# Performance work log

Measured on AMD Instinct MI355X. Metric: run time of the kernel, lower is better.

Reference implementation:

```python
import jax, jax.numpy as jnp
import numpy as np

N_NODES = 100000
N_EDGES = 1600000
NUM_FEATURES = 128
HIDDEN = 64
NUM_CLASSES = 16


def setup_inputs() -> dict:
    key = jax.random.key(0)
    k1, k2, k3, k4 = jax.random.split(key, 4)
    x = jax.random.normal(k1, (N_NODES, NUM_FEATURES), dtype=jnp.float32)
    edge_index = jax.random.randint(k2, (2, N_EDGES), 0, N_NODES, dtype=jnp.int64)
    # Glorot-ish scaled weights ([in, out] layout; PyG stores [out,in] but math is x @ W)
    W1 = jax.random.normal(k3, (NUM_FEATURES, HIDDEN), dtype=jnp.float32) * (1.0 / np.sqrt(NUM_FEATURES))
    W2 = jax.random.normal(k4, (HIDDEN, NUM_CLASSES), dtype=jnp.float32) * (1.0 / np.sqrt(HIDDEN))
    return {"x": x, "edge_index": edge_index, "W1": W1, "W2": W2}


def _gcn_conv(x, edge_index, W):
    # GCNConv(add_self_loops=False, bias=False): linear then sym-normalized scatter-add.
    n = x.shape[0]
    row, col = edge_index[0], edge_index[1]  # source -> target
    h = x @ W  # [N, out]
    # degree from unit edge weights scattered on target nodes
    deg = jax.ops.segment_sum(jnp.ones(row.shape[0], dtype=h.dtype), col, num_segments=n)
    deg_inv_sqrt = jnp.where(deg > 0, jax.lax.rsqrt(jnp.maximum(deg, 1.0)), 0.0)
    norm = deg_inv_sqrt[row] * deg_inv_sqrt[col]  # [E]
    msg = h[row] * norm[:, None]  # gather + scale, [E, out]
    return jax.ops.segment_sum(msg, col, num_segments=n)  # scatter-add to targets


def reference(x, edge_index, W1, W2):
    h = _gcn_conv(x, edge_index, W1)
    h = _gcn_conv(h, edge_index, W2)
    return jax.nn.log_softmax(h, axis=1)
```

## Files before the change

### kernel.cpp

```cpp
#include <hip/hip_runtime.h>
#include <hip/hip_bf16.h>
#include <hip/hip_fp16.h>


#define STRIDE 48
#define BCAP   3072


__global__ __launch_bounds__(512) void k_bucket(const int* __restrict__ ei,
                                                const void* __restrict__ xv,
                                                const void* __restrict__ W1v,
                                                const void* __restrict__ W2v,
                                                int* __restrict__ flags,
                                                float* __restrict__ W12,
                                                int* __restrict__ bcnt,
                                                int* __restrict__ buf,
                                                int e, int n, int nb) {
    __shared__ int hist[1024];
    __shared__ int basec[1024];
    __shared__ float wtmp[2048];
    __shared__ int sraw, sbad;
    int t = threadIdx.x;
    int b = blockIdx.x;

    if (t == 0) { sraw = 0; sbad = 0; }
    for (int i = t; i < nb; i += 512) hist[i] = 0;
    __syncthreads();

    {
        int i = b * 4096 + t;
        if (i < e && ei[2 * (size_t)i + 1] != 0) atomicOr(&sraw, 1);
    }
    if (b < 8) {
        const unsigned short* xs = (const unsigned short*)xv;
        int bad = 0;
        for (int i = t; i < 1024; i += 512) {
            unsigned ex2 = (xs[i] >> 7) & 0xFF;
            if (ex2 >= 0x90) bad = 1;
        }
        if (bad) atomicOr(&sbad, 1);
    }
    __syncthreads();
    int raw = sraw ? 0 : 1;

    if (b < 8) {
        bool f32 = sbad != 0;
        if (f32) {
            const float* W1 = (const float*)W1v;
            const float* W2 = (const float*)W2v;
            for (int i = t; i < 1024; i += 512) {
                wtmp[i] = W1[b * 1024 + i];
                wtmp[1024 + i] = W2[i];
            }
        } else {
            const __hip_bfloat16* W1 = (const __hip_bfloat16*)W1v;
            const __hip_bfloat16* W2 = (const __hip_bfloat16*)W2v;
            for (int i = t; i < 1024; i += 512) {
                wtmp[i] = __bfloat162float(W1[b * 1024 + i]);
                wtmp[1024 + i] = __bfloat162float(W2[i]);
            }
        }
    }

    int e0 = b * 4096;
    int bk[8], rec[8];
#pragma unroll
    for (int j = 0; j < 8; ++j) {
        int i = e0 + j * 512 + t;
        bk[j] = -1;
        if (i < e) {
            int r, c;
            if (raw) {
                r = ((const int2*)ei)[(size_t)i].x;
                c = ((const int2*)ei)[(size_t)e + i].x;
            } else {
                r = ei[i];
                c = ei[(size_t)e + i];
            }
            if ((unsigned)c < (unsigned)n && (unsigned)r < (unsigned)n) {
                bk[j] = c >> 7;
                rec[j] = ((c & 127) << 17) | r;
                atomicAdd(&hist[bk[j]], 1);
            }
        }
    }
    __syncthreads();

    if (b < 8 && t < 256) {
        int kl = t >> 4, c = t & 15;
        float acc = 0.0f;
#pragma unroll 8
        for (int f = 0; f < 64; ++f) acc += wtmp[kl * 64 + f] * wtmp[1024 + f * 16 + c];
        W12[(16 * b + kl) * 16 + c] = acc;
        if (b == 0 && t == 0) { flags[0] = sbad; flags[1] = raw; }
    }

    for (int i = t; i < nb; i += 512) {
        int h = hist[i];
        basec[i] = h ? atomicAdd(&bcnt[i], h) : 0;
    }
    __syncthreads();
#pragma unroll
    for (int j = 0; j < 8; ++j) {
        if (bk[j] >= 0) {
            int slot = atomicAdd(&basec[bk[j]], 1);
            if (slot < BCAP) buf[(size_t)bk[j] * BCAP + slot] = rec[j];
        }
    }
}


__global__ __launch_bounds__(256) void k_csr(const int* __restrict__ bcnt,
                                             const int* __restrict__ buf,
                                             int* __restrict__ cnt,
                                             int* __restrict__ csr, int n) {
    __shared__ int lcnt[128];
    __shared__ int lcsr[128 * STRIDE];
    int t = threadIdx.x;
    int b = blockIdx.x;
    if (t < 128) lcnt[t] = 0;
    int4 zero4 = {0, 0, 0, 0};
    for (int i = t; i < 128 * STRIDE / 4; i += 256) ((int4*)lcsr)[i] = zero4;
    __syncthreads();

    int m = bcnt[b];
    if (m > BCAP) m = BCAP;
    for (int i = t; i < m; i += 256) {
        int rec = buf[(size_t)b * BCAP + i];
        int cl = rec >> 17;
        int r = rec & 0x1FFFF;
        int slot = atomicAdd(&lcnt[cl], 1);
        if (slot < STRIDE) lcsr[cl * STRIDE + slot] = r;
    }
    __syncthreads();
    int node = (b << 7) + t;
    if (t < 128 && node < n) cnt[node] = lcnt[t];
    const int4* src = (const int4*)lcsr;
    int4* dst = (int4*)csr + (size_t)b * (128 * STRIDE / 4);
    for (int i = t; i < 128 * STRIDE / 4; i += 256) dst[i] = src[i];
}


__global__ __launch_bounds__(512) void k_z(const void* __restrict__ xv,
                                           const float* __restrict__ W12,
                                           const int* __restrict__ flags,
                                           const int* __restrict__ cnt,
                                           __half* __restrict__ z, int n) {
    __shared__ float part[4][128][17];
    int t = threadIdx.x;
    int b = blockIdx.x;
    int node_l = t & 127;
    int kq = t >> 7;
    int node0 = (b << 7) + node_l;
    int node = node0 < n ? node0 : n - 1;

    float acc[16];
#pragma unroll
    for (int c = 0; c < 16; ++c) acc[c] = 0.0f;

    if (flags[0]) {
        const float4* x4 = (const float4*)xv + (size_t)node * 32 + kq * 8;
#pragma unroll
        for (int j = 0; j < 8; ++j) {
            float4 v = x4[j];
            float xk[4] = {v.x, v.y, v.z, v.w};
#pragma unroll
            for (int q = 0; q < 4; ++q) {
                const float* w = &W12[(kq * 32 + j * 4 + q) * 16];
                float xx = xk[q];
#pragma unroll
                for (int c = 0; c < 16; ++c) acc[c] += xx * w[c];
            }
        }
    } else {
        const uint4* x4 = (const uint4*)xv + (size_t)node * 16 + kq * 4;
#pragma unroll
        for (int j = 0; j < 4; ++j) {
            uint4 v = x4[j];
            float xk[8];
            xk[0] = __uint_as_float(v.x << 16);
            xk[1] = __uint_as_float(v.x & 0xffff0000u);
            xk[2] = __uint_as_float(v.y << 16);
            xk[3] = __uint_as_float(v.y & 0xffff0000u);
            xk[4] = __uint_as_float(v.z << 16);
            xk[5] = __uint_as_float(v.z & 0xffff0000u);
            xk[6] = __uint_as_float(v.w << 16);
            xk[7] = __uint_as_float(v.w & 0xffff0000u);
#pragma unroll
            for (int q = 0; q < 8; ++q) {
                const float* w = &W12[(kq * 32 + j * 8 + q) * 16];
                float xx = xk[q];
#pragma unroll
                for (int c = 0; c < 16; ++c) acc[c] += xx * w[c];
            }
        }
    }

#pragma unroll
    for (int c = 0; c < 16; ++c) part[kq][node_l][c] = acc[c];
    __syncthreads();

    int nl2 = t >> 2;
    int cg = (t & 3) * 4;
    int node2 = (b << 7) + nl2;
    if (node2 < n) {
        float s0 = part[0][nl2][cg + 0] + part[1][nl2][cg + 0] + part[2][nl2][cg + 0] + part[3][nl2][cg + 0];
        float s1 = part[0][nl2][cg + 1] + part[1][nl2][cg + 1] + part[2][nl2][cg + 1] + part[3][nl2][cg + 1];
        float s2 = part[0][nl2][cg + 2] + part[1][nl2][cg + 2] + part[2][nl2][cg + 2] + part[3][nl2][cg + 2];
        float s3 = part[0][nl2][cg + 3] + part[1][nl2][cg + 3] + part[2][nl2][cg + 3] + part[3][nl2][cg + 3];
        int deg = cnt[node2];
        float di = (deg > 0) ? rsqrtf((float)deg) : 0.0f;
        __half2 h0 = __halves2half2(__float2half(s0 * di), __float2half(s1 * di));
        __half2 h1 = __halves2half2(__float2half(s2 * di), __float2half(s3 * di));
        uint2 u;
        u.x = *(unsigned*)&h0;
        u.y = *(unsigned*)&h1;
        ((uint2*)(z + (size_t)node2 * 16))[t & 3] = u;
    }
}


__global__ __launch_bounds__(256) void k_agg1b(const int* __restrict__ cnt,
                                               const int* __restrict__ csr,
                                               const __half* __restrict__ z,
                                               __half* __restrict__ z2, int n) {
    int t = threadIdx.x;
    int wid = t >> 6, lane = t & 63;
    int half = lane >> 5, l5 = lane & 31;
    int node0 = blockIdx.x * 8 + wid * 2 + half;
    int node = node0 < n ? node0 : n - 1;
    int id  = csr[(size_t)node * STRIDE + l5];
    int id2 = csr[(size_t)node * STRIDE + 32 + (l5 & 15)];
    int deg = cnt[node];
    float di = (deg > 0) ? rsqrtf((float)deg) : 0.0f;
    int m = deg < STRIDE ? deg : STRIDE;
    int sub = l5 >> 3, f2 = l5 & 7;
    int base = half << 5;
    const __half2* zp = (const __half2*)z;
    float ax = 0.0f, ay = 0.0f;
#pragma unroll
    for (int j = 0; j < 24; j += 4) {
        int s = __shfl(id, base + j + sub);
        float2 v = __half22float2(zp[(size_t)s * 8 + f2]);
        bool ok = (j + sub) < m;
        ax += ok ? v.x : 0.0f;
        ay += ok ? v.y : 0.0f;
    }
    for (int j = 24; j < m; j += 4) {
        int sidx = j + sub;
        int s = (j < 32) ? __shfl(id, base + sidx)
                         : __shfl(id2, base + (sidx & 15));
        if (sidx < m) {
            float2 v = __half22float2(zp[(size_t)s * 8 + f2]);
            ax += v.x;
            ay += v.y;
        }
    }
    ax += __shfl_xor(ax, 8);  ay += __shfl_xor(ay, 8);
    ax += __shfl_xor(ax, 16); ay += __shfl_xor(ay, 16);
    float s2 = di * di;
    if (node0 < n && l5 < 8)
        ((__half2*)z2)[(size_t)node * 8 + l5] =
            __halves2half2(__float2half(ax * s2), __float2half(ay * s2));
}


__global__ __launch_bounds__(256) void k_agg2b(const int* __restrict__ cnt,
                                               const int* __restrict__ csr,
                                               const __half* __restrict__ z2,
                                               const int* __restrict__ flags,
                                               void* __restrict__ outv, int n) {
    int t = threadIdx.x;
    int wid = t >> 6, lane = t & 63;
    int half = lane >> 5, l5 = lane & 31;
    int node0 = blockIdx.x * 8 + wid * 2 + half;
    int node = node0 < n ? node0 : n - 1;
    int id  = csr[(size_t)node * STRIDE + l5];
    int id2 = csr[(size_t)node * STRIDE + 32 + (l5 & 15)];
    int deg = cnt[node];
    float di = (deg > 0) ? rsqrtf((float)deg) : 0.0f;
    int m = deg < STRIDE ? deg : STRIDE;
    int sub = l5 >> 3, f2 = l5 & 7;
    int base = half << 5;
    const __half2* zp = (const __half2*)z2;
    float ax = 0.0f, ay = 0.0f;
#pragma unroll
    for (int j = 0; j < 24; j += 4) {
        int s = __shfl(id, base + j + sub);
        float2 v = __half22float2(zp[(size_t)s * 8 + f2]);
        bool ok = (j + sub) < m;
        ax += ok ? v.x : 0.0f;
        ay += ok ? v.y : 0.0f;
    }
    for (int j = 24; j < m; j += 4) {
        int sidx = j + sub;
        int s = (j < 32) ? __shfl(id, base + sidx)
                         : __shfl(id2, base + (sidx & 15));
        if (sidx < m) {
            float2 v = __half22float2(zp[(size_t)s * 8 + f2]);
            ax += v.x;
            ay += v.y;
        }
    }
    ax += __shfl_xor(ax, 8);  ay += __shfl_xor(ay, 8);
    ax += __shfl_xor(ax, 16); ay += __shfl_xor(ay, 16);
    float vx = ax * di, vy = ay * di;
    float mx = fmaxf(vx, vy);
#pragma unroll
    for (int d = 1; d <= 4; d <<= 1) mx = fmaxf(mx, __shfl_xor(mx, d));
    float es = __expf(vx - mx) + __expf(vy - mx);
#pragma unroll
    for (int d = 1; d <= 4; d <<= 1) es += __shfl_xor(es, d);
    float ls = __logf(es);
    float rx = vx - mx - ls, ry = vy - mx - ls;
    if (node0 < n && l5 < 8) {
        if (flags[0]) {
            float2 r; r.x = rx; r.y = ry;
            ((float2*)outv)[(size_t)node * 8 + l5] = r;
        } else {
            __hip_bfloat162 hh;
            hh.x = __float2bfloat16(rx);
            hh.y = __float2bfloat16(ry);
            ((__hip_bfloat162*)outv)[(size_t)node * 8 + l5] = hh;
        }
    }
}


extern "C" void kernel_launch(void* const* d_in, const int* in_sizes, int n_in,
                              void* d_out, int out_size, void* d_ws, size_t ws_size,
                              hipStream_t stream) {
    const int F = 128, C = 16;
    int n = in_sizes[0] / F;
    int e = in_sizes[1] / 2;
    int nb = (n + 127) >> 7;

    const void* x = d_in[0];
    const int* ei = (const int*)d_in[1];
    const void* W1 = d_in[2];
    const void* W2 = d_in[3];

    char* p = (char*)d_ws;
    auto carve = [&](size_t bytes) {
        char* r = p;
        p += (bytes + 255) & ~(size_t)255;
        return r;
    };
    int*    flags = (int*)  carve(256);
    int*    bcnt  = (int*)  carve((size_t)nb * 4);
    int*    cnt   = (int*)  carve((size_t)n * 4);
    float*  W12   = (float*)carve(128 * 16 * 4);
    int*    csr   = (int*)  carve(((size_t)nb * 128 * STRIDE + 64) * 4);
    __half* z     = (__half*)carve((size_t)n * C * 2);
    size_t buf_sz = (size_t)nb * BCAP * 4;
    size_t z2_sz = (size_t)n * C * 2;
    char* regionB = carve(buf_sz > z2_sz ? buf_sz : z2_sz);
    int*    buf = (int*)regionB;
    __half* z2  = (__half*)regionB;
    (void)ws_size;

    int gb_bucket = (e + 4095) / 4096;
    if (gb_bucket < 8) gb_bucket = 8;

    hipMemsetAsync(bcnt, 0, (size_t)nb * 4, stream);
    k_bucket<<<gb_bucket, 512, 0, stream>>>(ei, x, W1, W2, flags, W12, bcnt, buf, e, n, nb);
    k_csr<<<nb, 256, 0, stream>>>(bcnt, buf, cnt, csr, n);
    k_z<<<nb, 512, 0, stream>>>(x, W12, flags, cnt, z, n);
    k_agg1b<<<(n + 7) / 8, 256, 0, stream>>>(cnt, csr, z, z2, n);
    k_agg2b<<<(n + 7) / 8, 256, 0, stream>>>(cnt, csr, z2, flags, d_out, n);
}
```

Baseline: 193.1 us.

## Fuse projection kernel into CSR build and halve bucket block size

Merges the node projection (x @ W1W2 scaled by deg^-1/2) into the per-bucket CSR kernel, so the degree comes from shared memory and one kernel launch plus the cnt round-trip are removed. W12 is staged in shared memory. Each node now uses two threads that combine results with a shuffle, instead of four that reduce through shared memory. The bucketing kernel moves to 256-thread blocks covering 2048 edges each, which doubles the grid. The trade-off is heavier per-thread work and more register and shared-memory use in the fused kernel, with fewer threads per node for the x loads.

```diff
diff --git a/kernel.cpp b/kernel.cpp
--- a/kernel.cpp
+++ b/kernel.cpp
@@ -7,7 +7,7 @@
 #define BCAP   3072
 
 
-__global__ __launch_bounds__(512) void k_bucket(const int* __restrict__ ei,
+__global__ __launch_bounds__(256) void k_bucket(const int* __restrict__ ei,
                                                 const void* __restrict__ xv,
                                                 const void* __restrict__ W1v,
                                                 const void* __restrict__ W2v,
@@ -24,17 +24,17 @@
     int b = blockIdx.x;
 
     if (t == 0) { sraw = 0; sbad = 0; }
-    for (int i = t; i < nb; i += 512) hist[i] = 0;
+    for (int i = t; i < nb; i += 256) hist[i] = 0;
     __syncthreads();
 
     {
-        int i = b * 4096 + t;
+        int i = b * 2048 + t;
         if (i < e && ei[2 * (size_t)i + 1] != 0) atomicOr(&sraw, 1);
     }
     if (b < 8) {
         const unsigned short* xs = (const unsigned short*)xv;
         int bad = 0;
-        for (int i = t; i < 1024; i += 512) {
+        for (int i = t; i < 1024; i += 256) {
             unsigned ex2 = (xs[i] >> 7) & 0xFF;
             if (ex2 >= 0x90) bad = 1;
         }
@@ -48,25 +48,25 @@
         if (f32) {
             const float* W1 = (const float*)W1v;
             const float* W2 = (const float*)W2v;
-            for (int i = t; i < 1024; i += 512) {
+            for (int i = t; i < 1024; i += 256) {
                 wtmp[i] = W1[b * 1024 + i];
                 wtmp[1024 + i] = W2[i];
             }
         } else {
             const __hip_bfloat16* W1 = (const __hip_bfloat16*)W1v;
             const __hip_bfloat16* W2 = (const __hip_bfloat16*)W2v;
-            for (int i = t; i < 1024; i += 512) {
+            for (int i = t; i < 1024; i += 256) {
                 wtmp[i] = __bfloat162float(W1[b * 1024 + i]);
                 wtmp[1024 + i] = __bfloat162float(W2[i]);
             }
         }
     }
 
-    int e0 = b * 4096;
+    int e0 = b * 2048;
     int bk[8], rec[8];
 #pragma unroll
     for (int j = 0; j < 8; ++j) {
-        int i = e0 + j * 512 + t;
+        int i = e0 + j * 256 + t;
         bk[j] = -1;
         if (i < e) {
             int r, c;
@@ -86,7 +86,7 @@
     }
     __syncthreads();
 
-    if (b < 8 && t < 256) {
+    if (b < 8) {
         int kl = t >> 4, c = t & 15;
         float acc = 0.0f;
 #pragma unroll 8
@@ -95,7 +95,7 @@
         if (b == 0 && t == 0) { flags[0] = sbad; flags[1] = raw; }
     }
 
-    for (int i = t; i < nb; i += 512) {
+    for (int i = t; i < nb; i += 256) {
         int h = hist[i];
         basec[i] = h ? atomicAdd(&bcnt[i], h) : 0;
     }
@@ -110,17 +110,23 @@
 }
 
 
-__global__ __launch_bounds__(256) void k_csr(const int* __restrict__ bcnt,
-                                             const int* __restrict__ buf,
-                                             int* __restrict__ cnt,
-                                             int* __restrict__ csr, int n) {
+__global__ __launch_bounds__(256) void k_csr_z(const int* __restrict__ bcnt,
+                                               const int* __restrict__ buf,
+                                               const void* __restrict__ xv,
+                                               const float* __restrict__ W12,
+                                               const int* __restrict__ flags,
+                                               int* __restrict__ cnt,
+                                               int* __restrict__ csr,
+                                               __half* __restrict__ z, int n) {
     __shared__ int lcnt[128];
     __shared__ int lcsr[128 * STRIDE];
+    __shared__ float ws[2048];
     int t = threadIdx.x;
     int b = blockIdx.x;
     if (t < 128) lcnt[t] = 0;
     int4 zero4 = {0, 0, 0, 0};
     for (int i = t; i < 128 * STRIDE / 4; i += 256) ((int4*)lcsr)[i] = zero4;
+    for (int i = t; i < 2048; i += 256) ws[i] = W12[i];
     __syncthreads();
 
     int m = bcnt[b];
@@ -133,49 +139,43 @@
         if (slot < STRIDE) lcsr[cl * STRIDE + slot] = r;
     }
     __syncthreads();
-    int node = (b << 7) + t;
-    if (t < 128 && node < n) cnt[node] = lcnt[t];
+
+    {
+        int node = (b << 7) + t;
+        if (t < 128 && node < n) cnt[node] = lcnt[t];
+    }
     const int4* src = (const int4*)lcsr;
     int4* dst = (int4*)csr + (size_t)b * (128 * STRIDE / 4);
     for (int i = t; i < 128 * STRIDE / 4; i += 256) dst[i] = src[i];
-}
-
-
-__global__ __launch_bounds__(512) void k_z(const void* __restrict__ xv,
-                                           const float* __restrict__ W12,
-                                           const int* __restrict__ flags,
-                                           const int* __restrict__ cnt,
-                                           __half* __restrict__ z, int n) {
-    __shared__ float part[4][128][17];
-    int t = threadIdx.x;
-    int b = blockIdx.x;
-    int node_l = t & 127;
-    int kq = t >> 7;
+
+    int node_l = t >> 1;
+    int kh = t & 1;
     int node0 = (b << 7) + node_l;
-    int node = node0 < n ? node0 : n - 1;
+    if (node0 >= n) return;
+    int node = node0;
 
     float acc[16];
 #pragma unroll
     for (int c = 0; c < 16; ++c) acc[c] = 0.0f;
 
     if (flags[0]) {
-        const float4* x4 = (const float4*)xv + (size_t)node * 32 + kq * 8;
-#pragma unroll
-        for (int j = 0; j < 8; ++j) {
+        const float4* x4 = (const float4*)xv + (size_t)node * 32 + kh * 16;
+#pragma unroll
+        for (int j = 0; j < 16; ++j) {
             float4 v = x4[j];
             float xk[4] = {v.x, v.y, v.z, v.w};
 #pragma unroll
             for (int q = 0; q < 4; ++q) {
-                const float* w = &W12[(kq * 32 + j * 4 + q) * 16];
+                const float* w = &ws[(kh * 64 + j * 4 + q) * 16];
                 float xx = xk[q];
 #pragma unroll
                 for (int c = 0; c < 16; ++c) acc[c] += xx * w[c];
             }
         }
     } else {
-        const uint4* x4 = (const uint4*)xv + (size_t)node * 16 + kq * 4;
-#pragma unroll
-        for (int j = 0; j < 4; ++j) {
+        const uint4* x4 = (const uint4*)xv + (size_t)node * 16 + kh * 8;
+#pragma unroll
+        for (int j = 0; j < 8; ++j) {
             uint4 v = x4[j];
             float xk[8];
             xk[0] = __uint_as_float(v.x << 16);
@@ -188,7 +188,7 @@
             xk[7] = __uint_as_float(v.w & 0xffff0000u);
 #pragma unroll
             for (int q = 0; q < 8; ++q) {
-                const float* w = &W12[(kq * 32 + j * 8 + q) * 16];
+                const float* w = &ws[(kh * 64 + j * 8 + q) * 16];
                 float xx = xk[q];
 #pragma unroll
                 for (int c = 0; c < 16; ++c) acc[c] += xx * w[c];
@@ -197,26 +197,20 @@
     }
 
 #pragma unroll
-    for (int c = 0; c < 16; ++c) part[kq][node_l][c] = acc[c];
-    __syncthreads();
-
-    int nl2 = t >> 2;
-    int cg = (t & 3) * 4;
-    int node2 = (b << 7) + nl2;
-    if (node2 < n) {
-        float s0 = part[0][nl2][cg + 0] + part[1][nl2][cg + 0] + part[2][nl2][cg + 0] + part[3][nl2][cg + 0];
-        float s1 = part[0][nl2][cg + 1] + part[1][nl2][cg + 1] + part[2][nl2][cg + 1] + part[3][nl2][cg + 1];
-        float s2 = part[0][nl2][cg + 2] + part[1][nl2][cg + 2] + part[2][nl2][cg + 2] + part[3][nl2][cg + 2];
-        float s3 = part[0][nl2][cg + 3] + part[1][nl2][cg + 3] + part[2][nl2][cg + 3] + part[3][nl2][cg + 3];
-        int deg = cnt[node2];
-        float di = (deg > 0) ? rsqrtf((float)deg) : 0.0f;
-        __half2 h0 = __halves2half2(__float2half(s0 * di), __float2half(s1 * di));
-        __half2 h1 = __halves2half2(__float2half(s2 * di), __float2half(s3 * di));
-        uint2 u;
-        u.x = *(unsigned*)&h0;
-        u.y = *(unsigned*)&h1;
-        ((uint2*)(z + (size_t)node2 * 16))[t & 3] = u;
-    }
+    for (int c = 0; c < 16; ++c) acc[c] += __shfl_xor(acc[c], 1);
+
+    int deg = lcnt[node_l];
+    float di = (deg > 0) ? rsqrtf((float)deg) : 0.0f;
+    int c0 = kh * 8;
+    __half2 hh[4];
+#pragma unroll
+    for (int j = 0; j < 4; ++j)
+        hh[j] = __halves2half2(__float2half(acc[c0 + 2 * j] * di),
+                               __float2half(acc[c0 + 2 * j + 1] * di));
+    uint4 u;
+    u.x = *(unsigned*)&hh[0]; u.y = *(unsigned*)&hh[1];
+    u.z = *(unsigned*)&hh[2]; u.w = *(unsigned*)&hh[3];
+    ((uint4*)(z + (size_t)node * 16))[kh] = u;
 }
 
 
@@ -359,13 +353,12 @@
     __half* z2  = (__half*)regionB;
     (void)ws_size;
 
-    int gb_bucket = (e + 4095) / 4096;
+    int gb_bucket = (e + 2047) / 2048;
     if (gb_bucket < 8) gb_bucket = 8;
 
     hipMemsetAsync(bcnt, 0, (size_t)nb * 4, stream);
-    k_bucket<<<gb_bucket, 512, 0, stream>>>(ei, x, W1, W2, flags, W12, bcnt, buf, e, n, nb);
-    k_csr<<<nb, 256, 0, stream>>>(bcnt, buf, cnt, csr, n);
-    k_z<<<nb, 512, 0, stream>>>(x, W12, flags, cnt, z, n);
+    k_bucket<<<gb_bucket, 256, 0, stream>>>(ei, x, W1, W2, flags, W12, bcnt, buf, e, n, nb);
+    k_csr_z<<<nb, 256, 0, stream>>>(bcnt, buf, x, W12, flags, cnt, csr, z, n);
     k_agg1b<<<(n + 7) / 8, 256, 0, stream>>>(cnt, csr, z, z2, n);
     k_agg2b<<<(n + 7) / 8, 256, 0, stream>>>(cnt, csr, z2, flags, d_out, n);
 }
```

Result: faster. 181.0 us (-6.3%).
